# Optimization experiments

Hardware: AMD Instinct MI355X
Metric: run time of the kernel (lower is better)

The kernel has to match this reference:

```python
import jax, jax.numpy as jnp
import numpy as np

T, B, D_IN, D_H = 2048, 64, 256, 256


def setup_inputs() -> dict:
    key = jax.random.key(0)
    ks = jax.random.split(key, 6)
    s = 1.0 / np.sqrt(D_H)  # nn.RNNCell default init scale (uniform); use scaled normal for test data
    return {
        "x": jax.random.normal(ks[0], (T, B, D_IN), dtype=jnp.float32),
        "hx": jax.random.normal(ks[1], (B, D_H), dtype=jnp.float32),
        "W_ih": jax.random.normal(ks[2], (D_H, D_IN), dtype=jnp.float32) * s,
        "W_hh": jax.random.normal(ks[3], (D_H, D_H), dtype=jnp.float32) * s,
        "b_ih": jax.random.normal(ks[4], (D_H,), dtype=jnp.float32) * s,
        "b_hh": jax.random.normal(ks[5], (D_H,), dtype=jnp.float32) * s,
    }


def reference(x, hx, W_ih, W_hh, b_ih, b_hh):
    # RNNCell: h' = tanh(x_t @ W_ih^T + b_ih + h @ W_hh^T + b_hh)
    # Precompute the input projection for all timesteps in one big GEMM.
    xproj = jnp.einsum("tbi,hi->tbh", x, W_ih) + b_ih + b_hh  # [T, B, H]

    def step(h, xp_t):
        h_new = jnp.tanh(xp_t + h @ W_hh.T)
        return h_new, h_new

    h_last, outputs = jax.lax.scan(step, hx, xproj)
    return outputs, h_last  # outputs: [T, B, H] (stacked per-step hidden states)
```

## Files before the change

kernel.cpp:

```cpp
#include <hip/hip_runtime.h>
#include <hip/hip_bf16.h>

#define T_STEPS 2048
#define BATCH   64
#define DIN     256
#define DH      256

#define P1_BM 128
#define P1_BN 128
#define P1_KC 32
#define P1_PAD 4

__global__ __launch_bounds__(256) void xproj_kernel(
    const float* __restrict__ x, const float* __restrict__ W,
    const float* __restrict__ b_ih, const float* __restrict__ b_hh,
    float* __restrict__ out) {
  __shared__ float As[P1_KC][P1_BM + P1_PAD];
  __shared__ float Wt[P1_KC][P1_BN + P1_PAD];
  const int tid = threadIdx.x;
  const int m0 = blockIdx.x * P1_BM;
  const int j0 = blockIdx.y * P1_BN;
  const int r0 = (tid >> 4) * 8;
  const int c0 = (tid & 15) * 8;
  float acc[8][8] = {};

  for (int kc = 0; kc < DIN; kc += P1_KC) {
    __syncthreads();
#pragma unroll
    for (int s = 0; s < 4; ++s) {
      int idx = s * 256 + tid;
      int row = idx >> 3;
      int c4  = (idx & 7) << 2;
      float4 v = *reinterpret_cast<const float4*>(
          &x[(size_t)(m0 + row) * DIN + kc + c4]);
      As[c4 + 0][row] = v.x; As[c4 + 1][row] = v.y;
      As[c4 + 2][row] = v.z; As[c4 + 3][row] = v.w;
    }
#pragma unroll
    for (int s = 0; s < 4; ++s) {
      int idx = s * 256 + tid;
      int row = idx >> 3;
      int c4  = (idx & 7) << 2;
      float4 v = *reinterpret_cast<const float4*>(
          &W[(size_t)(j0 + row) * DIN + kc + c4]);
      Wt[c4 + 0][row] = v.x; Wt[c4 + 1][row] = v.y;
      Wt[c4 + 2][row] = v.z; Wt[c4 + 3][row] = v.w;
    }
    __syncthreads();
#pragma unroll
    for (int k = 0; k < P1_KC; ++k) {
      float4 a0 = *reinterpret_cast<const float4*>(&As[k][r0]);
      float4 a1 = *reinterpret_cast<const float4*>(&As[k][r0 + 4]);
      float4 w0 = *reinterpret_cast<const float4*>(&Wt[k][c0]);
      float4 w1 = *reinterpret_cast<const float4*>(&Wt[k][c0 + 4]);
      float a[8] = {a0.x, a0.y, a0.z, a0.w, a1.x, a1.y, a1.z, a1.w};
      float wv[8] = {w0.x, w0.y, w0.z, w0.w, w1.x, w1.y, w1.z, w1.w};
#pragma unroll
      for (int i = 0; i < 8; ++i)
#pragma unroll
        for (int jj = 0; jj < 8; ++jj)
          acc[i][jj] = fmaf(a[i], wv[jj], acc[i][jj]);
    }
  }

  float bias[8];
#pragma unroll
  for (int jj = 0; jj < 8; ++jj) bias[jj] = b_ih[j0 + c0 + jj] + b_hh[j0 + c0 + jj];
#pragma unroll
  for (int i = 0; i < 8; ++i) {
    size_t m = (size_t)(m0 + r0 + i);
#pragma unroll
    for (int j4 = 0; j4 < 2; ++j4) {
      float4 v;
      v.x = acc[i][j4 * 4 + 0] + bias[j4 * 4 + 0];
      v.y = acc[i][j4 * 4 + 1] + bias[j4 * 4 + 1];
      v.z = acc[i][j4 * 4 + 2] + bias[j4 * 4 + 2];
      v.w = acc[i][j4 * 4 + 3] + bias[j4 * 4 + 3];
      *reinterpret_cast<float4*>(&out[m * DH + j0 + c0 + j4 * 4]) = v;
    }
  }
}

__global__ __launch_bounds__(512) void rnn_scan_kernel(
    const float* __restrict__ hx, const float* __restrict__ W_hh,
    float* __restrict__ outbuf,
    float* __restrict__ hlast) {
  const int b    = blockIdx.x;
  const int tid  = threadIdx.x;
  const int wave = tid >> 6;
  const int lane = tid & 63;
  const int j    = wave * 32 + (lane & 31);
  const int kb   = (lane >> 5) * 128;

  float4 w[32];
#pragma unroll
  for (int i = 0; i < 32; ++i)
    w[i] = *reinterpret_cast<const float4*>(&W_hh[(size_t)j * DH + kb + i * 4]);

  __shared__ float h_lds[2][DH];
  if (tid < DH) h_lds[0][tid] = hx[(size_t)b * DH + tid];

  const size_t stride_t = (size_t)BATCH * DH;
  const size_t base     = (size_t)b * DH;

  float xp_next = outbuf[base + j];
  __syncthreads();

#pragma unroll 1
  for (int t = 0; t < T_STEPS; ++t) {
    const float xp = xp_next;
    if (t + 1 < T_STEPS)
      xp_next = outbuf[(size_t)(t + 1) * stride_t + base + j];

    const int cur = t & 1;
    const float4* __restrict__ hv =
        reinterpret_cast<const float4*>(&h_lds[cur][kb]);
    float p[8] = {};
#pragma unroll
    for (int i = 0; i < 32; ++i) {
      float4 h4 = hv[i];
      float a = p[i & 7];
      a = fmaf(w[i].x, h4.x, a);
      a = fmaf(w[i].y, h4.y, a);
      a = fmaf(w[i].z, h4.z, a);
      a = fmaf(w[i].w, h4.w, a);
      p[i & 7] = a;
    }
    float pa = ((p[0] + p[1]) + (p[2] + p[3])) + ((p[4] + p[5]) + (p[6] + p[7]));
    pa += __shfl_xor(pa, 32);

    const float s = pa + xp;
    const float e = __expf(2.0f * s);
    const float h = 1.0f - 2.0f * __builtin_amdgcn_rcpf(e + 1.0f);

    if ((lane >> 5) == 0) {
      h_lds[cur ^ 1][j] = h;
      outbuf[(size_t)t * stride_t + base + j] = h;
    }
    __syncthreads();
  }

  if (tid < DH) hlast[base + tid] = h_lds[0][tid];
}

extern "C" void kernel_launch(void* const* d_in, const int* in_sizes, int n_in,
                              void* d_out, int out_size, void* d_ws, size_t ws_size,
                              hipStream_t stream) {
  const float* x    = (const float*)d_in[0];
  const float* hx   = (const float*)d_in[1];
  const float* W_ih = (const float*)d_in[2];
  const float* W_hh = (const float*)d_in[3];
  const float* b_ih = (const float*)d_in[4];
  const float* b_hh = (const float*)d_in[5];
  float* out   = (float*)d_out;
  float* hlast = out + (size_t)T_STEPS * BATCH * DH;

  dim3 g1((T_STEPS * BATCH) / P1_BM, DH / P1_BN);
  xproj_kernel<<<g1, 256, 0, stream>>>(x, W_ih, b_ih, b_hh, out);

  rnn_scan_kernel<<<BATCH, 512, 0, stream>>>(hx, W_hh, out, hlast);
}
```

Measured before the change: 2.206 ms.

## Retile RNN scan matvec into 8x16 register blocks with butterfly shuffle reduction

Reorganizes the per-step W_hh·h matvec so each lane holds an 8-row by 16-column block of W_hh instead of one row half. Each lane then reads only 4 float4 values of h from a swizzled LDS layout instead of 32, which cuts LDS traffic per step. The 8 partial row sums are reduced across 16 lanes with a butterfly of xor shuffles that exchanges halves at each level. The cost is extra shuffles and selects on the serial critical path of every timestep.

```diff
diff --git a/kernel.cpp b/kernel.cpp
--- a/kernel.cpp
+++ b/kernel.cpp
@@ -89,58 +89,85 @@
   const int tid  = threadIdx.x;
   const int wave = tid >> 6;
   const int lane = tid & 63;
-  const int j    = wave * 32 + (lane & 31);
-  const int kb   = (lane >> 5) * 128;
+  const int kg   = lane & 15;
+  const int jg   = wave * 4 + (lane >> 4);
+  const int jred = jg * 8 + ((lane & 1) << 2) + (lane & 2) + ((lane >> 2) & 1);
 
-  float4 w[32];
+  float4 w[8][4];
 #pragma unroll
-  for (int i = 0; i < 32; ++i)
-    w[i] = *reinterpret_cast<const float4*>(&W_hh[(size_t)j * DH + kb + i * 4]);
+  for (int r = 0; r < 8; ++r)
+#pragma unroll
+    for (int c = 0; c < 4; ++c)
+      w[r][c] = *reinterpret_cast<const float4*>(
+          &W_hh[(size_t)(jg * 8 + r) * DH + kg * 16 + c * 4]);
 
-  __shared__ float h_lds[2][DH];
-  if (tid < DH) h_lds[0][tid] = hx[(size_t)b * DH + tid];
+  __shared__ float hbuf[2][4][16][4];
+  if (tid < DH) hbuf[0][(tid >> 2) & 3][tid >> 4][tid & 3] = hx[(size_t)b * DH + tid];
 
   const size_t stride_t = (size_t)BATCH * DH;
   const size_t base     = (size_t)b * DH;
 
-  float xp_next = outbuf[base + j];
+  float xp_next = outbuf[base + jred];
   __syncthreads();
 
 #pragma unroll 1
   for (int t = 0; t < T_STEPS; ++t) {
     const float xp = xp_next;
     if (t + 1 < T_STEPS)
-      xp_next = outbuf[(size_t)(t + 1) * stride_t + base + j];
+      xp_next = outbuf[(size_t)(t + 1) * stride_t + base + jred];
 
     const int cur = t & 1;
-    const float4* __restrict__ hv =
-        reinterpret_cast<const float4*>(&h_lds[cur][kb]);
-    float p[8] = {};
+    float4 hc[4];
 #pragma unroll
-    for (int i = 0; i < 32; ++i) {
-      float4 h4 = hv[i];
-      float a = p[i & 7];
-      a = fmaf(w[i].x, h4.x, a);
-      a = fmaf(w[i].y, h4.y, a);
-      a = fmaf(w[i].z, h4.z, a);
-      a = fmaf(w[i].w, h4.w, a);
-      p[i & 7] = a;
+    for (int c = 0; c < 4; ++c)
+      hc[c] = *reinterpret_cast<const float4*>(&hbuf[cur][c][kg][0]);
+
+    float p[8];
+#pragma unroll
+    for (int r = 0; r < 8; ++r) {
+      float a = 0.f;
+#pragma unroll
+      for (int c = 0; c < 4; ++c) {
+        a = fmaf(w[r][c].x, hc[c].x, a);
+        a = fmaf(w[r][c].y, hc[c].y, a);
+        a = fmaf(w[r][c].z, hc[c].z, a);
+        a = fmaf(w[r][c].w, hc[c].w, a);
+      }
+      p[r] = a;
     }
-    float pa = ((p[0] + p[1]) + (p[2] + p[3])) + ((p[4] + p[5]) + (p[6] + p[7]));
-    pa += __shfl_xor(pa, 32);
 
-    const float s = pa + xp;
+    const bool b0 = lane & 1, b1 = lane & 2, b2 = lane & 4;
+    float q[4];
+#pragma unroll
+    for (int i = 0; i < 4; ++i) {
+      float sent = b0 ? p[i] : p[4 + i];
+      float recv = __shfl_xor(sent, 1);
+      q[i] = (b0 ? p[4 + i] : p[i]) + recv;
+    }
+    float u[2];
+#pragma unroll
+    for (int i = 0; i < 2; ++i) {
+      float sent = b1 ? q[i] : q[2 + i];
+      float recv = __shfl_xor(sent, 2);
+      u[i] = (b1 ? q[2 + i] : q[i]) + recv;
+    }
+    float sent = b2 ? u[0] : u[1];
+    float v = (b2 ? u[1] : u[0]) + __shfl_xor(sent, 4);
+    v += __shfl_xor(v, 8);
+
+    const float s = v + xp;
     const float e = __expf(2.0f * s);
     const float h = 1.0f - 2.0f * __builtin_amdgcn_rcpf(e + 1.0f);
 
-    if ((lane >> 5) == 0) {
-      h_lds[cur ^ 1][j] = h;
-      outbuf[(size_t)t * stride_t + base + j] = h;
+    if (!(lane & 8)) {
+      hbuf[cur ^ 1][(jred >> 2) & 3][jred >> 4][jred & 3] = h;
+      outbuf[(size_t)t * stride_t + base + jred] = h;
     }
     __syncthreads();
   }
 
-  if (tid < DH) hlast[base + tid] = h_lds[0][tid];
+  if (tid < DH)
+    hlast[base + tid] = hbuf[0][(tid >> 2) & 3][tid >> 4][tid & 3];
 }
 
 extern "C" void kernel_launch(void* const* d_in, const int* in_sizes, int n_in,
```

Result: faster. 1.786 ms (-19.0%).
